# Kernel optimization log

Hardware: AMD Instinct MI355X
Metric: run time of the kernel (lower is better)

Reference implementation:

```python
import jax, jax.numpy as jnp
import numpy as np

HIDDEN = 1024
EMBED = 1024
SEQ = 512
BATCH = 64


def setup_inputs() -> dict:
    key = jax.random.key(0)
    k1, k2, k3 = jax.random.split(key, 3)
    factor = 1.0 / np.sqrt(HIDDEN)
    embeds = jax.random.normal(k1, (SEQ, BATCH, EMBED), dtype=jnp.float32)
    w = jax.random.uniform(k2, (HIDDEN + EMBED, 4 * HIDDEN), dtype=jnp.float32,
                           minval=-factor, maxval=factor)
    b = jax.random.uniform(k3, (4 * HIDDEN,), dtype=jnp.float32,
                           minval=-factor, maxval=factor)
    # forget-gate bias += 1 (gate order is g, i, f, o)
    b = b.at[2 * HIDDEN:3 * HIDDEN].add(1.0)
    return {"embeds": embeds, "w": w, "b": b}


def reference(embeds, w, b):
    T, B, E = embeds.shape
    H = w.shape[1] // 4

    def step(carry, x_t):
        h, c = carry
        data = jnp.concatenate([h, x_t], axis=-1)          # [B, H+E]
        big = data @ w + b                                  # [B, 4H]
        g, i, f, o = jnp.split(big, 4, axis=1)
        g = jnp.tanh(g)
        i = jax.nn.sigmoid(i)
        f = jax.nn.sigmoid(f)
        o = jax.nn.sigmoid(o)
        c_new = g * i + c * f
        h_new = jnp.tanh(c_new) * o
        return (h_new, c_new), h_new

    h0 = jnp.zeros((B, H), dtype=embeds.dtype)
    c0 = jnp.zeros((B, H), dtype=embeds.dtype)
    _, out = jax.lax.scan(step, (h0, c0), embeds)           # out: [T, B, H]
    return out
```

## Files before the change

### kernel.cpp

```cpp
#include <hip/hip_runtime.h>
#include <stdint.h>


#define TSTEPS 512
#define NBATCH 64
#define NHID   1024
#define NWG2   64
#define FLAGSTRIDE 32
#define AGENT  __HIP_MEMORY_SCOPE_AGENT

typedef __attribute__((ext_vector_type(8))) short bf16x8;
typedef __attribute__((ext_vector_type(4))) float f32x4;
typedef __attribute__((ext_vector_type(4))) int   i32x4;
typedef __attribute__((ext_vector_type(4))) float fl4;

__device__ __forceinline__ uint16_t f2bf(float f){
  uint32_t u = __float_as_uint(f);
  u += 0x7fffu + ((u >> 16) & 1u);
  return (uint16_t)(u >> 16);
}
__device__ __forceinline__ float bf2f(uint16_t b){
  return __uint_as_float(((uint32_t)b) << 16);
}
__device__ __forceinline__ float sigm(float x){ return 1.0f/(1.0f + __expf(-x)); }
__device__ __forceinline__ float tanhfast(float x){ return 1.0f - 2.0f/(__expf(2.0f*x) + 1.0f); }
__device__ __forceinline__ bf16x8 as_bf(i32x4 v){
  union { i32x4 i; bf16x8 b; } u; u.i = v; return u.b;
}

__global__ void k0a_cvt(const float* __restrict__ in, uint16_t* __restrict__ outp, int n8){
  int stride = gridDim.x * blockDim.x;
  for (int i = blockIdx.x * blockDim.x + threadIdx.x; i < n8; i += stride){
    const fl4* p = (const fl4*)(in + (size_t)i * 8);
    fl4 v0 = p[0], v1 = p[1];
    union { uint16_t u[8]; i32x4 v; } r;
    r.u[0]=f2bf(v0.x); r.u[1]=f2bf(v0.y); r.u[2]=f2bf(v0.z); r.u[3]=f2bf(v0.w);
    r.u[4]=f2bf(v1.x); r.u[5]=f2bf(v1.y); r.u[6]=f2bf(v1.z); r.u[7]=f2bf(v1.w);
    *(i32x4*)(outp + (size_t)i * 8) = r.v;
  }
}

__global__ void k0b_trans(const float* __restrict__ w, uint16_t* __restrict__ wT){
  __shared__ float tile[64 * 65];
  int k0 = blockIdx.x * 64;
  int n0 = blockIdx.y * 64;
  int tid = threadIdx.x;
  int r  = tid >> 2;
  int cq = (tid & 3) * 16;
#pragma unroll
  for (int i = 0; i < 4; ++i){
    fl4 v = *(const fl4*)(w + (size_t)(k0 + r) * 4096 + n0 + cq + i * 4);
    tile[r*65 + cq + i*4 + 0] = v.x;
    tile[r*65 + cq + i*4 + 1] = v.y;
    tile[r*65 + cq + i*4 + 2] = v.z;
    tile[r*65 + cq + i*4 + 3] = v.w;
  }
  __syncthreads();
  union { uint16_t u[8]; i32x4 v; } a, b;
#pragma unroll
  for (int i = 0; i < 8; ++i) a.u[i] = f2bf(tile[(cq + i) * 65 + r]);
#pragma unroll
  for (int i = 0; i < 8; ++i) b.u[i] = f2bf(tile[(cq + 8 + i) * 65 + r]);
  *(i32x4*)(wT + (size_t)(n0 + r) * 2048 + k0 + cq)     = a.v;
  *(i32x4*)(wT + (size_t)(n0 + r) * 2048 + k0 + cq + 8) = b.v;
}

__launch_bounds__(256, 2)
__global__ void k1_xw(const uint16_t* __restrict__ ebf, const uint16_t* __restrict__ wT,
                      const float* __restrict__ bias, uint16_t* __restrict__ xw){
  __shared__ char sm[32768];
  char* As = sm;
  char* Bs = sm + 16384;
  int bid = blockIdx.x;
  int nt = bid & 31, mt = bid >> 5;
  int m0 = mt * 128, n0 = nt * 128;
  int tid = threadIdx.x;
  int lane = tid & 63, wid = tid >> 6;
  int wr = wid >> 1, wc = wid & 1;

  f32x4 zero = {0.f, 0.f, 0.f, 0.f};
  f32x4 acc[4][4];
#pragma unroll
  for (int mi = 0; mi < 4; ++mi)
#pragma unroll
    for (int ni = 0; ni < 4; ++ni) acc[mi][ni] = zero;

  for (int kt = 0; kt < 16; ++kt){
    __syncthreads();
#pragma unroll
    for (int i = 0; i < 4; ++i){
      int L = i * 256 + tid;
      int row = L >> 3, c = L & 7;
      i32x4 va = *(const i32x4*)(ebf + (size_t)(m0 + row) * 1024 + kt * 64 + c * 8);
      *(i32x4*)(As + row * 128 + ((c ^ (row & 7)) * 16)) = va;
      i32x4 vb = *(const i32x4*)(wT + (size_t)(n0 + row) * 2048 + 1024 + kt * 64 + c * 8);
      *(i32x4*)(Bs + row * 128 + ((c ^ (row & 7)) * 16)) = vb;
    }
    __syncthreads();
#pragma unroll
    for (int kk = 0; kk < 2; ++kk){
      bf16x8 a[4], b[4];
      int ci = kk * 4 + (lane >> 4);
#pragma unroll
      for (int mi = 0; mi < 4; ++mi){
        int rl = wr * 64 + mi * 16 + (lane & 15);
        a[mi] = *(const bf16x8*)(As + rl * 128 + ((ci ^ (rl & 7)) * 16));
      }
#pragma unroll
      for (int ni = 0; ni < 4; ++ni){
        int sl = wc * 64 + ni * 16 + (lane & 15);
        b[ni] = *(const bf16x8*)(Bs + sl * 128 + ((ci ^ (sl & 7)) * 16));
      }
#pragma unroll
      for (int mi = 0; mi < 4; ++mi)
#pragma unroll
        for (int ni = 0; ni < 4; ++ni)
          acc[mi][ni] = __builtin_amdgcn_mfma_f32_16x16x32_bf16(a[mi], b[ni], acc[mi][ni], 0, 0, 0);
    }
  }
  float bcol[4];
#pragma unroll
  for (int ni = 0; ni < 4; ++ni) bcol[ni] = bias[n0 + wc * 64 + ni * 16 + (lane & 15)];
#pragma unroll
  for (int mi = 0; mi < 4; ++mi)
#pragma unroll
    for (int ni = 0; ni < 4; ++ni)
#pragma unroll
      for (int jj = 0; jj < 4; ++jj){
        int rg = m0 + wr * 64 + mi * 16 + (lane >> 4) * 4 + jj;
        int cg = n0 + wc * 64 + ni * 16 + (lane & 15);
        xw[(size_t)rg * 4096 + cg] = f2bf(acc[mi][ni][jj] + bcol[ni]);
      }
}

#define LDA(k, OFF) asm volatile("global_load_dwordx4 %0, %1, off offset:" #OFF " sc0 sc1" \
                                 : "=v"(ap[k]) : "v"(aB) : "memory")
#define WAITV(N) do { asm volatile("s_waitcnt vmcnt(" #N ")" ::: "memory"); \
                      __builtin_amdgcn_sched_barrier(0); } while(0)
#define GBLK(K0) \
  _Pragma("unroll") \
  for (int kc = K0; kc < K0 + 8; ++kc){ \
    bf16x8 a = as_bf(ap[kc]); \
    _Pragma("unroll") \
    for (int g = 0; g < 4; ++g){ \
      bf16x8 b = *(const bf16x8*)(WP + ((kc * 4 + g) << 10) + (lane << 4)); \
      acc[g] = __builtin_amdgcn_mfma_f32_16x16x32_bf16(a, b, acc[g], 0, 0, 0); \
    } \
  }

__launch_bounds__(256, 1)
__global__ void k2_rec(const uint16_t* __restrict__ xw, const uint16_t* __restrict__ wT,
                       uint16_t* __restrict__ hbuf, int* __restrict__ flags,
                       float* __restrict__ outp){
  extern __shared__ char sm[];
  char* WP = sm;

  int tid  = threadIdx.x;
  int lane = tid & 63;
  int wid  = tid >> 6;
  int wg = blockIdx.x;
  int j0 = wg * 16;

#pragma unroll
  for (int i = 0; i < 32; ++i){
    int L = i * 256 + tid;
    int kc = L >> 8;
    int g  = (L >> 6) & 3;
    int l6 = L & 63;
    int q  = (l6 >> 4) & 3;
    int rr = l6 & 15;
    i32x4 v = *(const i32x4*)(wT + (size_t)(g * 1024 + j0 + rr) * 2048 + kc * 32 + q * 8);
    *(i32x4*)(WP + (size_t)L * 16) = v;
  }
  __syncthreads();

  const int r0 = wid * 16;
  const int q  = lane >> 4;
  const int rr = lane & 15;

  float creg[4] = {0.f, 0.f, 0.f, 0.f};

  uint16_t xc[4][4];
  {
    const uint16_t* xp = xw + (size_t)0 * (64 * 4096) + j0 + rr;
#pragma unroll
    for (int g = 0; g < 4; ++g)
#pragma unroll
      for (int p = 0; p < 4; ++p)
        xc[g][p] = xp[(size_t)(r0 + q * 4 + p) * 4096 + g * 1024];
  }

  for (int t = 0; t < TSTEPS; ++t){
    if (t > 0){
      if (tid < 64){
        while (true){
          int v = __hip_atomic_load(&flags[tid * FLAGSTRIDE], __ATOMIC_RELAXED, AGENT);
          if (__all(v >= t)) break;
          __builtin_amdgcn_s_sleep(1);
        }
      }
      __syncthreads();
    }

    const uint16_t* hsrc = hbuf + (size_t)t * (NBATCH * NHID);
    const uint16_t* aB = hsrc + (size_t)(r0 + rr) * 1024 + q * 8;
    i32x4 ap[32];
    LDA(0,0);     LDA(1,64);    LDA(2,128);   LDA(3,192);
    LDA(4,256);   LDA(5,320);   LDA(6,384);   LDA(7,448);
    LDA(8,512);   LDA(9,576);   LDA(10,640);  LDA(11,704);
    LDA(12,768);  LDA(13,832);  LDA(14,896);  LDA(15,960);
    LDA(16,1024); LDA(17,1088); LDA(18,1152); LDA(19,1216);
    LDA(20,1280); LDA(21,1344); LDA(22,1408); LDA(23,1472);
    LDA(24,1536); LDA(25,1600); LDA(26,1664); LDA(27,1728);
    LDA(28,1792); LDA(29,1856); LDA(30,1920); LDA(31,1984);

    uint16_t xn[4][4];
    {
      int tn = (t < TSTEPS - 1) ? t + 1 : t;
      const uint16_t* xp = xw + (size_t)tn * (64 * 4096) + j0 + rr;
#pragma unroll
      for (int g = 0; g < 4; ++g)
#pragma unroll
        for (int p = 0; p < 4; ++p)
          xn[g][p] = xp[(size_t)(r0 + q * 4 + p) * 4096 + g * 1024];
    }

    f32x4 acc[4];
#pragma unroll
    for (int g = 0; g < 4; ++g) acc[g] = (f32x4){0.f, 0.f, 0.f, 0.f};

    WAITV(40); GBLK(0);
    WAITV(32); GBLK(8);
    WAITV(24); GBLK(16);
    WAITV(16); GBLK(24);

    uint16_t* hdst = hbuf + (size_t)(t + 1) * (NBATCH * NHID);
    float*    odst = outp + (size_t)t * (NBATCH * NHID);
#pragma unroll
    for (int p = 0; p < 4; ++p){
      int row = r0 + q * 4 + p;
      float G = acc[0][p] + bf2f(xc[0][p]);
      float I = acc[1][p] + bf2f(xc[1][p]);
      float F = acc[2][p] + bf2f(xc[2][p]);
      float O = acc[3][p] + bf2f(xc[3][p]);
      G = tanhfast(G); I = sigm(I); F = sigm(F); O = sigm(O);
      float c = G * I + creg[p] * F;
      creg[p] = c;
      float h = tanhfast(c) * O;
      size_t idx = (size_t)row * 1024 + j0 + rr;
      odst[idx] = h;
      __hip_atomic_store(hdst + idx, f2bf(h), __ATOMIC_RELAXED, AGENT);
    }

#pragma unroll
    for (int g = 0; g < 4; ++g)
#pragma unroll
      for (int p = 0; p < 4; ++p)
        xc[g][p] = xn[g][p];

    asm volatile("s_waitcnt vmcnt(0)" ::: "memory");
    __syncthreads();
    if (tid == 0)
      __hip_atomic_store(&flags[wg * FLAGSTRIDE], t + 1, __ATOMIC_RELAXED, AGENT);
  }
}

extern "C" void kernel_launch(void* const* d_in, const int* in_sizes, int n_in,
                              void* d_out, int out_size, void* d_ws, size_t ws_size,
                              hipStream_t stream){
  const float* embeds = (const float*)d_in[0];
  const float* w      = (const float*)d_in[1];
  const float* bias   = (const float*)d_in[2];
  float* outp = (float*)d_out;
  char* ws = (char*)d_ws;

  const size_t o_ebf = 0;
  const size_t o_wT  = o_ebf + (size_t)32768 * 1024 * 2;
  const size_t o_xw  = o_wT  + (size_t)4096 * 2048 * 2;
  const size_t o_hb  = o_xw  + (size_t)32768 * 4096 * 2;
  const size_t o_fl  = o_hb  + (size_t)513 * 64 * 1024 * 2;

  uint16_t* ebf  = (uint16_t*)(ws + o_ebf);
  uint16_t* wT   = (uint16_t*)(ws + o_wT);
  uint16_t* xw   = (uint16_t*)(ws + o_xw);
  uint16_t* hbuf = (uint16_t*)(ws + o_hb);
  int*      flags= (int*)(ws + o_fl);

  hipMemsetAsync(ws + o_hb, 0, (size_t)64 * 1024 * 2, stream);
  hipMemsetAsync(ws + o_fl, 0, NWG2 * FLAGSTRIDE * sizeof(int), stream);

  k0a_cvt<<<2048, 256, 0, stream>>>(embeds, ebf, (512 * 64 * 1024) / 8);
  k0b_trans<<<dim3(32, 64), 256, 0, stream>>>(w, wT);
  k1_xw<<<8192, 256, 0, stream>>>(ebf, wT, bias, xw);

  (void)hipFuncSetAttribute((const void*)k2_rec,
                            hipFuncAttributeMaxDynamicSharedMemorySize, 131072);
  k2_rec<<<NWG2, 256, 131072, stream>>>(xw, wT, hbuf, flags, outp);
}
```

Baseline: 4.560 ms.

## Use per-wave flags, defer fp32 output to a separate pass, deepen x prefetch

The block-wide barrier and single per-workgroup flag are replaced by per-wave flags. Each wave polls only the 64 flags of the matching wave index in every workgroup, so waves advance independently. The fp32 output store is removed from the sequential recurrence, and a new kernel writes the output afterwards by widening the bf16 h history to fp32. The xw prefetch now runs two steps ahead with nontemporal accesses, and the sc0/sc1 cache-bypass bits are dropped from the h loads. Dropping those bits risks reading stale h values across L2 domains, and the output now carries bf16 rounding instead of fp32.

```diff
diff --git a/kernel.cpp b/kernel.cpp
--- a/kernel.cpp
+++ b/kernel.cpp
@@ -129,11 +129,12 @@
       for (int jj = 0; jj < 4; ++jj){
         int rg = m0 + wr * 64 + mi * 16 + (lane >> 4) * 4 + jj;
         int cg = n0 + wc * 64 + ni * 16 + (lane & 15);
-        xw[(size_t)rg * 4096 + cg] = f2bf(acc[mi][ni][jj] + bcol[ni]);
-      }
-}
-
-#define LDA(k, OFF) asm volatile("global_load_dwordx4 %0, %1, off offset:" #OFF " sc0 sc1" \
+        __builtin_nontemporal_store(f2bf(acc[mi][ni][jj] + bcol[ni]),
+                                    &xw[(size_t)rg * 4096 + cg]);
+      }
+}
+
+#define LDA(k, OFF) asm volatile("global_load_dwordx4 %0, %1, off offset:" #OFF \
                                  : "=v"(ap[k]) : "v"(aB) : "memory")
 #define WAITV(N) do { asm volatile("s_waitcnt vmcnt(" #N ")" ::: "memory"); \
                       __builtin_amdgcn_sched_barrier(0); } while(0)
@@ -157,7 +158,7 @@
 
   int tid  = threadIdx.x;
   int lane = tid & 63;
-  int wid  = tid >> 6;
+  int w    = tid >> 6;
   int wg = blockIdx.x;
   int j0 = wg * 16;
 
@@ -167,39 +168,40 @@
     int kc = L >> 8;
     int g  = (L >> 6) & 3;
     int l6 = L & 63;
-    int q  = (l6 >> 4) & 3;
-    int rr = l6 & 15;
-    i32x4 v = *(const i32x4*)(wT + (size_t)(g * 1024 + j0 + rr) * 2048 + kc * 32 + q * 8);
+    int q_ = (l6 >> 4) & 3;
+    int rr_ = l6 & 15;
+    i32x4 v = *(const i32x4*)(wT + (size_t)(g * 1024 + j0 + rr_) * 2048 + kc * 32 + q_ * 8);
     *(i32x4*)(WP + (size_t)L * 16) = v;
   }
   __syncthreads();
 
-  const int r0 = wid * 16;
+  const int r0 = w * 16;
   const int q  = lane >> 4;
   const int rr = lane & 15;
 
   float creg[4] = {0.f, 0.f, 0.f, 0.f};
 
-  uint16_t xc[4][4];
+  uint16_t xc[4][4], xn[4][4];
   {
-    const uint16_t* xp = xw + (size_t)0 * (64 * 4096) + j0 + rr;
+    const uint16_t* xp0 = xw + j0 + rr;
+    const uint16_t* xp1 = xw + (size_t)1 * (64 * 4096) + j0 + rr;
 #pragma unroll
     for (int g = 0; g < 4; ++g)
 #pragma unroll
-      for (int p = 0; p < 4; ++p)
-        xc[g][p] = xp[(size_t)(r0 + q * 4 + p) * 4096 + g * 1024];
+      for (int p = 0; p < 4; ++p){
+        xc[g][p] = xp0[(size_t)(r0 + q * 4 + p) * 4096 + g * 1024];
+        xn[g][p] = xp1[(size_t)(r0 + q * 4 + p) * 4096 + g * 1024];
+      }
   }
 
   for (int t = 0; t < TSTEPS; ++t){
     if (t > 0){
-      if (tid < 64){
-        while (true){
-          int v = __hip_atomic_load(&flags[tid * FLAGSTRIDE], __ATOMIC_RELAXED, AGENT);
-          if (__all(v >= t)) break;
-          __builtin_amdgcn_s_sleep(1);
-        }
-      }
-      __syncthreads();
+      int fi = (lane * 4 + w) * FLAGSTRIDE;
+      while (true){
+        int v = __hip_atomic_load(&flags[fi], __ATOMIC_RELAXED, AGENT);
+        if (__all(v >= t)) break;
+        __builtin_amdgcn_s_sleep(1);
+      }
     }
 
     const uint16_t* hsrc = hbuf + (size_t)t * (NBATCH * NHID);
@@ -214,15 +216,16 @@
     LDA(24,1536); LDA(25,1600); LDA(26,1664); LDA(27,1728);
     LDA(28,1792); LDA(29,1856); LDA(30,1920); LDA(31,1984);
 
-    uint16_t xn[4][4];
+    uint16_t xn2[4][4];
     {
-      int tn = (t < TSTEPS - 1) ? t + 1 : t;
+      int tn = (t < TSTEPS - 2) ? t + 2 : TSTEPS - 1;
       const uint16_t* xp = xw + (size_t)tn * (64 * 4096) + j0 + rr;
 #pragma unroll
       for (int g = 0; g < 4; ++g)
 #pragma unroll
         for (int p = 0; p < 4; ++p)
-          xn[g][p] = xp[(size_t)(r0 + q * 4 + p) * 4096 + g * 1024];
+          xn2[g][p] = __builtin_nontemporal_load(
+                        &xp[(size_t)(r0 + q * 4 + p) * 4096 + g * 1024]);
     }
 
     f32x4 acc[4];
@@ -235,10 +238,8 @@
     WAITV(16); GBLK(24);
 
     uint16_t* hdst = hbuf + (size_t)(t + 1) * (NBATCH * NHID);
-    float*    odst = outp + (size_t)t * (NBATCH * NHID);
 #pragma unroll
     for (int p = 0; p < 4; ++p){
-      int row = r0 + q * 4 + p;
       float G = acc[0][p] + bf2f(xc[0][p]);
       float I = acc[1][p] + bf2f(xc[1][p]);
       float F = acc[2][p] + bf2f(xc[2][p]);
@@ -247,21 +248,34 @@
       float c = G * I + creg[p] * F;
       creg[p] = c;
       float h = tanhfast(c) * O;
-      size_t idx = (size_t)row * 1024 + j0 + rr;
-      odst[idx] = h;
-      __hip_atomic_store(hdst + idx, f2bf(h), __ATOMIC_RELAXED, AGENT);
-    }
+      __hip_atomic_store(hdst + (size_t)(r0 + q * 4 + p) * 1024 + j0 + rr,
+                         f2bf(h), __ATOMIC_RELAXED, AGENT);
+    }
+
+    asm volatile("s_waitcnt vmcnt(0)" ::: "memory");
+    if (lane == 0)
+      __hip_atomic_store(&flags[(wg * 4 + w) * FLAGSTRIDE], t + 1, __ATOMIC_RELAXED, AGENT);
 
 #pragma unroll
     for (int g = 0; g < 4; ++g)
 #pragma unroll
-      for (int p = 0; p < 4; ++p)
+      for (int p = 0; p < 4; ++p){
         xc[g][p] = xn[g][p];
-
-    asm volatile("s_waitcnt vmcnt(0)" ::: "memory");
-    __syncthreads();
-    if (tid == 0)
-      __hip_atomic_store(&flags[wg * FLAGSTRIDE], t + 1, __ATOMIC_RELAXED, AGENT);
+        xn[g][p] = xn2[g][p];
+      }
+  }
+}
+
+__global__ void k3_out(const uint16_t* __restrict__ hb, float* __restrict__ outp, int n8){
+  int stride = gridDim.x * blockDim.x;
+  for (int i = blockIdx.x * blockDim.x + threadIdx.x; i < n8; i += stride){
+    i32x4 v = *(const i32x4*)(hb + (size_t)(NBATCH * NHID) + (size_t)i * 8);
+    const uint16_t* u = (const uint16_t*)&v;
+    fl4 o0, o1;
+    o0.x = bf2f(u[0]); o0.y = bf2f(u[1]); o0.z = bf2f(u[2]); o0.w = bf2f(u[3]);
+    o1.x = bf2f(u[4]); o1.y = bf2f(u[5]); o1.z = bf2f(u[6]); o1.w = bf2f(u[7]);
+    __builtin_nontemporal_store(o0, (fl4*)(outp + (size_t)i * 8));
+    __builtin_nontemporal_store(o1, (fl4*)(outp + (size_t)i * 8 + 4));
   }
 }
 
@@ -287,7 +301,7 @@
   int*      flags= (int*)(ws + o_fl);
 
   hipMemsetAsync(ws + o_hb, 0, (size_t)64 * 1024 * 2, stream);
-  hipMemsetAsync(ws + o_fl, 0, NWG2 * FLAGSTRIDE * sizeof(int), stream);
+  hipMemsetAsync(ws + o_fl, 0, 256 * FLAGSTRIDE * sizeof(int), stream);
 
   k0a_cvt<<<2048, 256, 0, stream>>>(embeds, ebf, (512 * 64 * 1024) / 8);
   k0b_trans<<<dim3(32, 64), 256, 0, stream>>>(w, wT);
@@ -296,4 +310,6 @@
   (void)hipFuncSetAttribute((const void*)k2_rec,
                             hipFuncAttributeMaxDynamicSharedMemorySize, 131072);
   k2_rec<<<NWG2, 256, 131072, stream>>>(xw, wT, hbuf, flags, outp);
-}
+
+  k3_out<<<2048, 256, 0, stream>>>(hbuf, outp, (512 * 64 * 1024) / 8);
+}
```

Measured after the change: 4.474 ms. Within noise of the previous version (-1.9%).
